# Performance work log

Hardware: AMD Instinct MI355X
Metric: run time of the kernel (lower is better)

Reference implementation:

```python
import jax, jax.numpy as jnp
import numpy as np
import math

H = 1024
N = 64          # d_state; complex modes = N // 2
N2 = N // 2
B = 8
L = 2048
DT_MIN, DT_MAX = 0.001, 0.1


def setup_inputs() -> dict:
    key = jax.random.key(0)
    ks = jax.random.split(key, 8)
    u = jax.random.normal(ks[0], (B, H, L), dtype=jnp.float32)
    # log_dt ~ Uniform[log(dt_min), log(dt_max)]
    log_dt = (jax.random.uniform(ks[1], (H,), dtype=jnp.float32)
              * (math.log(DT_MAX) - math.log(DT_MIN)) + math.log(DT_MIN))
    # random_dplr with scaling='inverse': real part 0.5, imag = (1/pi)*N*(N/(1+2n)-1)
    n = jnp.arange(N2, dtype=jnp.float32)
    w_real = 0.5 * jnp.ones((1, N2), dtype=jnp.float32)
    w_imag = ((1.0 / math.pi) * N * (N / (1.0 + 2.0 * n) - 1.0))[None, :].astype(jnp.float32)
    log_w_real = jnp.log(w_real + 1e-4)  # module stores log(-w.real + 1e-4)
    # C = randn complex (channels=1, H, N2), scaled by normalized B (folded into randn here)
    C_re = jax.random.normal(ks[2], (1, H, N2), dtype=jnp.float32) / math.sqrt(2 * N2)
    C_im = jax.random.normal(ks[3], (1, H, N2), dtype=jnp.float32) / math.sqrt(2 * N2)
    D = jax.random.normal(ks[4], (1, H), dtype=jnp.float32)
    # output_linear: Conv1d(k=1) from channels*H -> H  => weight (H, H)
    W_out = jax.random.normal(ks[5], (H, H), dtype=jnp.float32) / math.sqrt(H)
    b_out = jax.random.normal(ks[6], (H,), dtype=jnp.float32) * 0.01
    return {"u": u, "log_dt": log_dt, "log_w_real": log_w_real, "w_imag": w_imag,
            "C_re": C_re, "C_im": C_im, "D": D, "W_out": W_out, "b_out": b_out}


def reference(u, log_dt, log_w_real, w_imag, C_re, C_im, D, W_out, b_out):
    b, h, l = u.shape
    # --- SSKernelDiag.forward ---
    dt = jnp.exp(log_dt)                                   # (H,)
    w = -jnp.exp(log_w_real) + 1j * w_imag                 # (n_ssm=1, N2)
    w = jnp.broadcast_to(w, (h, w.shape[-1]))              # repeat copies -> (H, N2)
    dtA = w * dt[:, None]                                  # (H, N2) complex
    C = (C_re + 1j * C_im) * (jnp.exp(dtA) - 1.0) / w      # (c, H, N2)
    # Vandermonde: exp(dtA * arange(L)) -> (H, N2, L) complex
    K = jnp.exp(dtA[:, :, None] * jnp.arange(l, dtype=jnp.float32))
    k = 2.0 * jnp.einsum('chn,hnl->chl', C, K).real        # (c, H, L) float
    # --- FFT convolution ---
    k_f = jnp.fft.rfft(k, n=2 * l)                         # (c, H, L+1)
    u_f = jnp.fft.rfft(u, n=2 * l)                         # (B, H, L+1)
    y_f = jnp.einsum('bhl,chl->bchl', u_f, k_f)
    y = jnp.fft.irfft(y_f, n=2 * l)[..., :l]               # (B, c, H, L)
    # skip connection with D
    y = y + jnp.einsum('bhl,ch->bchl', u, D)
    y = y.reshape(b, -1, l)                                # (B, c*H, L)
    y = jax.nn.gelu(y, approximate=False)
    # output 1x1 conv: (B, c*H, L) x (H, c*H) -> (B, H, L)
    y = jnp.einsum('bil,oi->bol', y, W_out) + b_out[None, :, None]
    return y
```

## Files before the change

### kernel.cpp

```cpp
#include <hip/hip_runtime.h>
#include <hip/hip_bf16.h>

#define HH 1024
#define LL 2048
#define BB 8
#define NN2 32
#define CT 128
#define NCH 16

typedef short bf16x8 __attribute__((ext_vector_type(8)));
typedef float f32x4  __attribute__((ext_vector_type(4)));

static __device__ __forceinline__ unsigned short bfbits(float x) {
    __hip_bfloat16 h = __float2bfloat16(x);
    return *(unsigned short*)&h;
}
static __device__ __forceinline__ float f_from_bits(unsigned short b) {
    __hip_bfloat16 h; *(unsigned short*)&h = b; return __bfloat162float(h);
}
static __device__ __forceinline__ float2 cexp_n(float2 dA, float p) {
    float mag = __expf(dA.x * p);
    float rev = dA.y * p * 0.15915494309f;
    rev -= floorf(rev);
    float ang = rev * 6.28318530718f;
    return make_float2(mag * __cosf(ang), mag * __sinf(ang));
}

#define SWZ(off, row) ((off) ^ (((row) & 7) << 4))

__global__ __launch_bounds__(256) void aux_tables(
    const float* __restrict__ log_dt, const float* __restrict__ log_w_real,
    const float* __restrict__ w_imag, const float* __restrict__ C_re,
    const float* __restrict__ C_im,
    __hip_bfloat16* __restrict__ AJ_g, __hip_bfloat16* __restrict__ AP_g,
    float* __restrict__ misc_g)
{
    __shared__ float2 dtA_s[NN2];
    __shared__ float2 Cn_s[NN2];
    const int tid = threadIdx.x;
    const int h = blockIdx.x;

    if (tid < NN2) {
        int n = tid;
        float dt = expf(log_dt[h]);
        float wr = -expf(log_w_real[n]);
        float wi = w_imag[n];
        float dar = wr * dt, dai = wi * dt;
        dtA_s[n] = make_float2(dar, dai);
        float er = expf(dar);
        float sn, cs; sincosf(dai, &sn, &cs);
        float exr = er * cs - 1.0f, exi = er * sn;
        float den = wr * wr + wi * wi;
        float fr = (exr * wr + exi * wi) / den;
        float fi = (exi * wr - exr * wi) / den;
        float cre = C_re[h * NN2 + n], cim = C_im[h * NN2 + n];
        float2 Cv = make_float2(cre * fr - cim * fi, cre * fi + cim * fr);
        Cn_s[n] = Cv;
        misc_g[h * 256 + 128 + 2 * n]     = Cv.x;
        misc_g[h * 256 + 128 + 2 * n + 1] = Cv.y;
        float magA = expf(dar * 128.0f);
        float snA, csA; sincosf(dai * 128.0f, &snA, &csA);
        misc_g[h * 256 + 192 + 2 * n]     = magA * csA;
        misc_g[h * 256 + 192 + 2 * n + 1] = magA * snA;
    }
    __syncthreads();

    char* ajb = (char*)AJ_g + (size_t)h * 16384;
    #pragma unroll
    for (int q = 0; q < 2; ++q) {
        int task = q * 256 + tid;
        int n = task >> 4, j0 = (task & 15) * 8;
        float2 dA = dtA_s[n];
        unsigned rw[4], iw[4];
        #pragma unroll
        for (int i2 = 0; i2 < 4; ++i2) {
            float2 a0 = cexp_n(dA, (float)(127 - j0 - 2 * i2));
            float2 a1 = cexp_n(dA, (float)(127 - j0 - 2 * i2 - 1));
            rw[i2] = (unsigned)bfbits(a0.x) | ((unsigned)bfbits(a1.x) << 16);
            iw[i2] = (unsigned)bfbits(a0.y) | ((unsigned)bfbits(a1.y) << 16);
        }
        int r0 = 2 * n, r1 = 2 * n + 1;
        *(uint4*)(ajb + SWZ(r0 * 256 + j0 * 2, r0)) = make_uint4(rw[0], rw[1], rw[2], rw[3]);
        *(uint4*)(ajb + SWZ(r1 * 256 + j0 * 2, r1)) = make_uint4(iw[0], iw[1], iw[2], iw[3]);
    }

    char* apb = (char*)AP_g + (size_t)h * 16384;
    #pragma unroll
    for (int q = 0; q < 2; ++q) {
        int task = q * 256 + tid;
        int ttr = task >> 2, n0 = (task & 3) * 8;
        unsigned w[8];
        #pragma unroll
        for (int i = 0; i < 8; ++i) {
            float2 a = cexp_n(dtA_s[n0 + i], (float)(ttr + 1));
            w[i] = (unsigned)bfbits(2.0f * a.x) | ((unsigned)bfbits(-2.0f * a.y) << 16);
        }
        *(uint4*)(apb + SWZ(ttr * 128 + n0 * 4, ttr))      = make_uint4(w[0], w[1], w[2], w[3]);
        *(uint4*)(apb + SWZ(ttr * 128 + n0 * 4 + 16, ttr)) = make_uint4(w[4], w[5], w[6], w[7]);
    }

    {
        int t = tid >> 1, nb = (tid & 1) * 16;
        float s = 0.f;
        #pragma unroll
        for (int i = 0; i < 16; ++i) {
            int n = nb + i;
            float2 a = cexp_n(dtA_s[n], (float)t);
            float2 C = Cn_s[n];
            s += C.x * a.x - C.y * a.y;
        }
        s += __shfl_xor(s, 1);
        if ((tid & 1) == 0) misc_g[h * 256 + t] = 2.0f * s;
    }
}

#define S_U    0
#define S_UN   32768
#define S_P    49152
#define S_KT   65536
#define S_TOT  66560

#define KBUILD(hf)                                                       \
    _Pragma("unroll")                                                    \
    for (int q = 0; q < 4; ++q) {                                        \
        int idx = q * 512 + tid;                                         \
        int ttr = idx >> 4, j0 = (idx & 15) * 4;                         \
        int base = ttr - (hf) * 64 - j0;                                 \
        ushort4 o;                                                       \
        o.x = (base     >= 0) ? bfbits(kt[base])     : (unsigned short)0;\
        o.y = (base - 1 >= 0) ? bfbits(kt[base - 1]) : (unsigned short)0;\
        o.z = (base - 2 >= 0) ? bfbits(kt[base - 2]) : (unsigned short)0;\
        o.w = (base - 3 >= 0) ? bfbits(kt[base - 3]) : (unsigned short)0;\
        *(ushort4*)(smem + SWZ(S_UN + ttr * 128 + j0 * 2, ttr)) = o;     \
    }

__global__ __launch_bounds__(512, 4) void ssm_mfma(
    const float* __restrict__ u,
    const __hip_bfloat16* __restrict__ AJ_g,
    const __hip_bfloat16* __restrict__ AP_g,
    const float* __restrict__ misc_g,
    const float* __restrict__ Dp, __hip_bfloat16* __restrict__ g_out)
{
    extern __shared__ char smem[];
    float*  kt   = (float*)(smem + S_KT);
    float2* CnL  = (float2*)(smem + S_KT + 512);
    float2* A128 = (float2*)(smem + S_KT + 768);

    const int tid  = threadIdx.x;
    const int lane = tid & 63;
    const int wave = tid >> 6;
    const int wr4  = wave >> 1;
    const int wc2  = wave & 1;
    const int h    = blockIdx.x;

    {
        const char* ajs = (const char*)AJ_g + (size_t)h * 16384;
        __builtin_amdgcn_global_load_lds(
            (const __attribute__((address_space(1))) void*)(ajs + tid * 16),
            (__attribute__((address_space(3))) void*)(smem + S_UN + wave * 1024), 16, 0, 0);
        __builtin_amdgcn_global_load_lds(
            (const __attribute__((address_space(1))) void*)(ajs + 8192 + tid * 16),
            (__attribute__((address_space(3))) void*)(smem + S_UN + 8192 + wave * 1024), 16, 0, 0);
        if (tid < 64) {
            const char* ms = (const char*)misc_g + (size_t)h * 1024;
            __builtin_amdgcn_global_load_lds(
                (const __attribute__((address_space(1))) void*)(ms + tid * 16),
                (__attribute__((address_space(3))) void*)(smem + S_KT), 16, 0, 0);
        }
    }

    float4 ureg[8];
    #pragma unroll
    for (int q = 0; q < 8; ++q)
        ureg[q] = *(const float4*)(u + ((size_t)(q * HH + h)) * LL + tid * 4);
    #pragma unroll
    for (int q = 0; q < 8; ++q) {
        int row = q * 16 + (tid >> 5);
        int j   = (tid & 31) * 4;
        ushort4 o;
        o.x = bfbits(ureg[q].x); o.y = bfbits(ureg[q].y);
        o.z = bfbits(ureg[q].z); o.w = bfbits(ureg[q].w);
        *(ushort4*)(smem + SWZ(S_U + row * 256 + j * 2, row)) = o;
    }
    asm volatile("s_waitcnt vmcnt(0)" ::: "memory");
    __syncthreads();

    f32x4 accP[2][2] = {};
    #pragma unroll
    for (int ks = 0; ks < 4; ++ks) {
        int kf = ks * 32 + (lane >> 4) * 8;
        bf16x8 a0, a1, b0, b1;
        {
            int r = wr4 * 32 + (lane & 15);
            a0 = *(bf16x8*)(smem + SWZ(S_U + r * 256 + kf * 2, r));
            int r2 = r + 16;
            a1 = *(bf16x8*)(smem + SWZ(S_U + r2 * 256 + kf * 2, r2));
        }
        {
            int r = wc2 * 32 + (lane & 15);
            b0 = *(bf16x8*)(smem + SWZ(S_UN + r * 256 + kf * 2, r));
            int r2 = r + 16;
            b1 = *(bf16x8*)(smem + SWZ(S_UN + r2 * 256 + kf * 2, r2));
        }
        accP[0][0] = __builtin_amdgcn_mfma_f32_16x16x32_bf16(a0, b0, accP[0][0], 0, 0, 0);
        accP[0][1] = __builtin_amdgcn_mfma_f32_16x16x32_bf16(a0, b1, accP[0][1], 0, 0, 0);
        accP[1][0] = __builtin_amdgcn_mfma_f32_16x16x32_bf16(a1, b0, accP[1][0], 0, 0, 0);
        accP[1][1] = __builtin_amdgcn_mfma_f32_16x16x32_bf16(a1, b1, accP[1][1], 0, 0, 0);
    }
    #pragma unroll
    for (int mt = 0; mt < 2; ++mt)
        #pragma unroll
        for (int nt = 0; nt < 2; ++nt)
            #pragma unroll
            for (int r = 0; r < 4; ++r) {
                int row = wr4 * 32 + mt * 16 + (lane >> 4) * 4 + r;
                int col = wc2 * 32 + nt * 16 + (lane & 15);
                *(unsigned short*)(smem + SWZ(S_P + row * 128 + col * 2, row)) =
                    bfbits(accP[mt][nt][r]);
            }
    __syncthreads();

    KBUILD(0)
    if (tid < 256) {
        int b = tid >> 5, n = tid & 31;
        float2 C = CnL[n];
        float2 A = A128[n];
        float sr = 0.f, si = 0.f;
        for (int c = 0; c < NCH; ++c) {
            int row = b * 16 + c;
            int off = SWZ(S_P + row * 128 + n * 4, row);
            unsigned int pv = *(unsigned int*)(smem + off);
            float pr = f_from_bits((unsigned short)(pv & 0xffff));
            float pi = f_from_bits((unsigned short)(pv >> 16));
            float csr = C.x * sr - C.y * si;
            float csi = C.x * si + C.y * sr;
            *(unsigned int*)(smem + off) =
                (unsigned)bfbits(csr) | ((unsigned)bfbits(csi) << 16);
            float nsr = A.x * sr - A.y * si + pr;
            float nsi = A.x * si + A.y * sr + pi;
            sr = nsr; si = nsi;
        }
    }
    __syncthreads();

    f32x4 acc[2][4] = {};
    #pragma unroll
    for (int ks = 0; ks < 2; ++ks) {
        int kf = ks * 32 + (lane >> 4) * 8;
        bf16x8 a0, a1, bv[4];
        {
            int r = wr4 * 32 + (lane & 15);
            a0 = *(bf16x8*)(smem + SWZ(S_U + r * 256 + kf * 2, r));
            int r2 = r + 16;
            a1 = *(bf16x8*)(smem + SWZ(S_U + r2 * 256 + kf * 2, r2));
        }
        #pragma unroll
        for (int nt = 0; nt < 4; ++nt) {
            int ttr = wc2 * 64 + nt * 16 + (lane & 15);
            bv[nt] = *(bf16x8*)(smem + SWZ(S_UN + ttr * 128 + kf * 2, ttr));
        }
        #pragma unroll
        for (int nt = 0; nt < 4; ++nt) {
            acc[0][nt] = __builtin_amdgcn_mfma_f32_16x16x32_bf16(a0, bv[nt], acc[0][nt], 0, 0, 0);
            acc[1][nt] = __builtin_amdgcn_mfma_f32_16x16x32_bf16(a1, bv[nt], acc[1][nt], 0, 0, 0);
        }
    }
    __syncthreads();

    KBUILD(1)
    __syncthreads();
    #pragma unroll
    for (int ks = 0; ks < 2; ++ks) {
        int kf = ks * 32 + (lane >> 4) * 8;
        bf16x8 a0, a1, bv[4];
        {
            int r = wr4 * 32 + (lane & 15);
            a0 = *(bf16x8*)(smem + SWZ(S_U + r * 256 + 128 + kf * 2, r));
            int r2 = r + 16;
            a1 = *(bf16x8*)(smem + SWZ(S_U + r2 * 256 + 128 + kf * 2, r2));
        }
        #pragma unroll
        for (int nt = 0; nt < 4; ++nt) {
            int ttr = wc2 * 64 + nt * 16 + (lane & 15);
            bv[nt] = *(bf16x8*)(smem + SWZ(S_UN + ttr * 128 + kf * 2, ttr));
        }
        #pragma unroll
        for (int nt = 0; nt < 4; ++nt) {
            acc[0][nt] = __builtin_amdgcn_mfma_f32_16x16x32_bf16(a0, bv[nt], acc[0][nt], 0, 0, 0);
            acc[1][nt] = __builtin_amdgcn_mfma_f32_16x16x32_bf16(a1, bv[nt], acc[1][nt], 0, 0, 0);
        }
    }
    __syncthreads();

    {
        const char* aps = (const char*)AP_g + (size_t)h * 16384;
        __builtin_amdgcn_global_load_lds(
            (const __attribute__((address_space(1))) void*)(aps + tid * 16),
            (__attribute__((address_space(3))) void*)(smem + S_UN + wave * 1024), 16, 0, 0);
        __builtin_amdgcn_global_load_lds(
            (const __attribute__((address_space(1))) void*)(aps + 8192 + tid * 16),
            (__attribute__((address_space(3))) void*)(smem + S_UN + 8192 + wave * 1024), 16, 0, 0);
    }
    asm volatile("s_waitcnt vmcnt(0)" ::: "memory");
    __syncthreads();

    #pragma unroll
    for (int ks = 0; ks < 2; ++ks) {
        int kf = ks * 32 + (lane >> 4) * 8;
        bf16x8 a0, a1, bv[4];
        {
            int r = wr4 * 32 + (lane & 15);
            a0 = *(bf16x8*)(smem + SWZ(S_P + r * 128 + kf * 2, r));
            int r2 = r + 16;
            a1 = *(bf16x8*)(smem + SWZ(S_P + r2 * 128 + kf * 2, r2));
        }
        #pragma unroll
        for (int nt = 0; nt < 4; ++nt) {
            int ttr = wc2 * 64 + nt * 16 + (lane & 15);
            bv[nt] = *(bf16x8*)(smem + SWZ(S_UN + ttr * 128 + kf * 2, ttr));
        }
        #pragma unroll
        for (int nt = 0; nt < 4; ++nt) {
            acc[0][nt] = __builtin_amdgcn_mfma_f32_16x16x32_bf16(a0, bv[nt], acc[0][nt], 0, 0, 0);
            acc[1][nt] = __builtin_amdgcn_mfma_f32_16x16x32_bf16(a1, bv[nt], acc[1][nt], 0, 0, 0);
        }
    }

    const float Dv = Dp[h];
    #pragma unroll
    for (int mt = 0; mt < 2; ++mt)
        #pragma unroll
        for (int nt = 0; nt < 4; ++nt)
            #pragma unroll
            for (int r = 0; r < 4; ++r) {
                int row = wr4 * 32 + mt * 16 + (lane >> 4) * 4 + r;
                int ttr = wc2 * 64 + nt * 16 + (lane & 15);
                int off = SWZ(S_U + row * 256 + ttr * 2, row);
                float uv = f_from_bits(*(unsigned short*)(smem + off));
                float y = acc[mt][nt][r] + Dv * uv;
                float z = 0.7978845608f * (y + 0.044715f * y * y * y);
                float e = __expf(2.0f * z);
                float th = 1.0f - 2.0f / (e + 1.0f);
                float gel = 0.5f * y * (1.0f + th);
                *(unsigned short*)(smem + off) = bfbits(gel);
            }
    __syncthreads();
    #pragma unroll
    for (int q = 0; q < 4; ++q) {
        int flat = q * 512 + tid;
        int row = flat >> 4, c16 = flat & 15;
        uint4 v = *(uint4*)(smem + SWZ(S_U + row * 256 + c16 * 16, row));
        int b = row >> 4, c = row & 15;
        *(uint4*)(g_out + ((size_t)(b * HH + h)) * LL + c * CT + c16 * 8) = v;
    }
}

__global__ __launch_bounds__(256) void conv_w(
    const float* __restrict__ W, __hip_bfloat16* __restrict__ Wb)
{
    int i = blockIdx.x * 256 + threadIdx.x;
    float4 v = ((const float4*)W)[i];
    ushort4 o;
    o.x = bfbits(v.x); o.y = bfbits(v.y); o.z = bfbits(v.z); o.w = bfbits(v.w);
    ((ushort4*)Wb)[i] = o;
}

__global__ __launch_bounds__(256) void transpose_g(
    const __hip_bfloat16* __restrict__ g, __hip_bfloat16* __restrict__ gT)
{
    __shared__ __hip_bfloat16 t[64][66];
    const int tid = threadIdx.x;
    const int b  = blockIdx.z;
    const int h0 = blockIdx.x * 64;
    const int l0 = blockIdx.y * 64;

    #pragma unroll
    for (int q = 0; q < 2; ++q) {
        int idx = tid + q * 256;
        int r = idx >> 3, c8 = (idx & 7) * 8;
        uint4 v = *(const uint4*)(g + ((size_t)(b * HH + h0 + r)) * LL + l0 + c8);
        unsigned int* dst = (unsigned int*)&t[r][c8];
        dst[0] = v.x; dst[1] = v.y; dst[2] = v.z; dst[3] = v.w;
    }
    __syncthreads();
    #pragma unroll
    for (int q = 0; q < 2; ++q) {
        int idx = tid + q * 256;
        int r = idx >> 3, c8 = (idx & 7) * 8;
        unsigned short tmp[8];
        #pragma unroll
        for (int j = 0; j < 8; ++j) tmp[j] = *(unsigned short*)&t[c8 + j][r];
        uint4 o;
        o.x = (unsigned)tmp[0] | ((unsigned)tmp[1] << 16);
        o.y = (unsigned)tmp[2] | ((unsigned)tmp[3] << 16);
        o.z = (unsigned)tmp[4] | ((unsigned)tmp[5] << 16);
        o.w = (unsigned)tmp[6] | ((unsigned)tmp[7] << 16);
        *(uint4*)(gT + ((size_t)(b * LL + l0 + r)) * HH + h0 + c8) = o;
    }
}

#define GSLOT 32768
#define STAGE_TILE(kt_, s_)                                                      \
    {                                                                            \
        const int k0_ = (kt_) * 64;                                              \
        _Pragma("unroll")                                                        \
        for (int v_ = 0; v_ < 4; ++v_) {                                         \
            int row_ = v_ * 64 + rsub;                                           \
            const __hip_bfloat16* ga_ = Wb + (size_t)(o0 + row_) * HH + k0_ + csw; \
            const __hip_bfloat16* gb_ = gT + (size_t)(n0 + row_) * HH + k0_ + csw; \
            char* dA_ = smem + (s_) * GSLOT + (v_ * 64 + wave * 8) * 128;        \
            char* dB_ = smem + 2 * GSLOT + (s_) * GSLOT + (v_ * 64 + wave * 8) * 128; \
            __builtin_amdgcn_global_load_lds(                                    \
                (const __attribute__((address_space(1))) void*)ga_,              \
                (__attribute__((address_space(3))) void*)dA_, 16, 0, 0);         \
            __builtin_amdgcn_global_load_lds(                                    \
                (const __attribute__((address_space(1))) void*)gb_,              \
                (__attribute__((address_space(3))) void*)dB_, 16, 0, 0);         \
        }                                                                        \
    }

#define COMPUTE_TILE(s_)                                                         \
    {                                                                            \
        const char* baseA = smem + (s_) * GSLOT;                                 \
        const char* baseB = smem + 2 * GSLOT + (s_) * GSLOT;                     \
        bf16x8 bfr[4][2];                                                        \
        _Pragma("unroll")                                                        \
        for (int nt = 0; nt < 4; ++nt)                                           \
            _Pragma("unroll")                                                    \
            for (int ks = 0; ks < 2; ++ks) {                                     \
                int rb = wn * 64 + nt * 16 + (lane & 15);                        \
                int c  = (ks * 32 + (lane >> 4) * 8) ^ ((rb & 7) << 3);          \
                bfr[nt][ks] = *(const bf16x8*)(baseB + rb * 128 + c * 2);        \
            }                                                                    \
        _Pragma("unroll")                                                        \
        for (int qq = 0; qq < 4; ++qq) {                                         \
            bf16x8 af[2][2];                                                     \
            _Pragma("unroll")                                                    \
            for (int mt = 0; mt < 2; ++mt)                                       \
                _Pragma("unroll")                                                \
                for (int ks = 0; ks < 2; ++ks) {                                 \
                    int ra = wm * 128 + (qq * 2 + mt) * 16 + (lane & 15);        \
                    int c  = (ks * 32 + (lane >> 4) * 8) ^ ((ra & 7) << 3);      \
                    af[mt][ks] = *(const bf16x8*)(baseA + ra * 128 + c * 2);     \
                }                                                                \
            __builtin_amdgcn_s_setprio(1);                                       \
            _Pragma("unroll")                                                    \
            for (int mt = 0; mt < 2; ++mt)                                       \
                _Pragma("unroll")                                                \
                for (int nt = 0; nt < 4; ++nt) {                                 \
                    acc[qq * 2 + mt][nt] = __builtin_amdgcn_mfma_f32_16x16x32_bf16( \
                        af[mt][0], bfr[nt][0], acc[qq * 2 + mt][nt], 0, 0, 0);   \
                    acc[qq * 2 + mt][nt] = __builtin_amdgcn_mfma_f32_16x16x32_bf16( \
                        af[mt][1], bfr[nt][1], acc[qq * 2 + mt][nt], 0, 0, 0);   \
                }                                                                \
            __builtin_amdgcn_s_setprio(0);                                       \
        }                                                                        \
    }

__global__ __launch_bounds__(512, 2) void out_gemm_256(
    const __hip_bfloat16* __restrict__ Wb,
    const __hip_bfloat16* __restrict__ gT,
    const float* __restrict__ bias,
    float* __restrict__ out)
{
    extern __shared__ char smem[];
    const int tid  = threadIdx.x;
    const int lane = tid & 63;
    const int wave = tid >> 6;
    const int wm = wave >> 2;
    const int wn = wave & 3;

    int wg  = blockIdx.x;
    int swz = (wg & 7) * 32 + (wg >> 3);
    const int o0 = (swz & 3) * 256;
    const int n0 = (swz >> 2) * 256;

    const int rsub = tid >> 3;
    const int csw  = ((tid & 7) ^ (rsub & 7)) << 3;

    f32x4 acc[8][4] = {};

    STAGE_TILE(0, 0)
    STAGE_TILE(1, 1)

    for (int t = 0; t < 15; ++t) {
        asm volatile("s_waitcnt vmcnt(8)" ::: "memory");
        __builtin_amdgcn_s_barrier();
        __builtin_amdgcn_sched_barrier(0);
        COMPUTE_TILE(t & 1)
        asm volatile("s_waitcnt lgkmcnt(0)" ::: "memory");
        __builtin_amdgcn_s_barrier();
        __builtin_amdgcn_sched_barrier(0);
        if (t < 14) STAGE_TILE(t + 2, t & 1)
    }
    asm volatile("s_waitcnt vmcnt(0)" ::: "memory");
    __builtin_amdgcn_s_barrier();
    __builtin_amdgcn_sched_barrier(0);
    COMPUTE_TILE(1)

    const int bb = n0 >> 11;
    #pragma unroll
    for (int m = 0; m < 8; ++m) {
        int o = o0 + wm * 128 + m * 16 + (lane >> 4) * 4;
        #pragma unroll
        for (int nt = 0; nt < 4; ++nt) {
            int n = n0 + wn * 64 + nt * 16 + (lane & 15);
            int l = n & 2047;
            #pragma unroll
            for (int r = 0; r < 4; ++r)
                out[((size_t)(bb * HH + o + r)) * LL + l] = acc[m][nt][r] + bias[o + r];
        }
    }
}

extern "C" void kernel_launch(void* const* d_in, const int* in_sizes, int n_in,
                              void* d_out, int out_size, void* d_ws, size_t ws_size,
                              hipStream_t stream) {
    const float* u          = (const float*)d_in[0];
    const float* log_dt     = (const float*)d_in[1];
    const float* log_w_real = (const float*)d_in[2];
    const float* w_imag     = (const float*)d_in[3];
    const float* C_re       = (const float*)d_in[4];
    const float* C_im       = (const float*)d_in[5];
    const float* Dp         = (const float*)d_in[6];
    const float* W          = (const float*)d_in[7];
    const float* bias       = (const float*)d_in[8];
    float* out = (float*)d_out;

    __hip_bfloat16* AJ_g = (__hip_bfloat16*)d_out;
    __hip_bfloat16* AP_g = (__hip_bfloat16*)((char*)d_out + 16777216);
    __hip_bfloat16* g    = (__hip_bfloat16*)((char*)d_out + 33554432);
    __hip_bfloat16* gT     = (__hip_bfloat16*)d_ws;
    __hip_bfloat16* Wb     = (__hip_bfloat16*)((char*)d_ws + 33554432);
    float*          misc_g = (float*)((char*)d_ws + 35651584);

    hipFuncSetAttribute((const void*)ssm_mfma,
                        hipFuncAttributeMaxDynamicSharedMemorySize, S_TOT);
    hipFuncSetAttribute((const void*)out_gemm_256,
                        hipFuncAttributeMaxDynamicSharedMemorySize, 131072);

    conv_w<<<dim3(HH * HH / 1024), 256, 0, stream>>>(W, Wb);
    aux_tables<<<dim3(HH), 256, 0, stream>>>(log_dt, log_w_real, w_imag,
                                             C_re, C_im, AJ_g, AP_g, misc_g);
    ssm_mfma<<<dim3(HH), 512, S_TOT, stream>>>(u, AJ_g, AP_g, misc_g, Dp, g);
    transpose_g<<<dim3(HH / 64, LL / 64, BB), 256, 0, stream>>>(g, gT);
    out_gemm_256<<<dim3(256), 512, 131072, stream>>>(Wb, gT, bias, out);
}
```

Measured before the change: 107.6 us.

## Replace Toeplitz KBUILD with shifted kernel rows, fuse weight conversion, prefetch AP early

Instead of materialising the 128x128 Toeplitz block of the SSM kernel twice (KBUILD for each half), each wave builds one of 8 shifted, reversed copies of the kernel, and the MFMA B operands are read straight from those padded rows. This removes two block-wide syncs and one of the two half passes of the intra-chunk GEMM. The AP_g async global-to-LDS load now starts before the state scan, so it overlaps with that work. The separate fp32-to-bf16 weight conversion kernel is folded into aux_tables, which removes one launch. LDS use grows slightly, and the unswizzled padded-row reads may cause bank conflicts.

```diff
diff --git a/kernel.cpp b/kernel.cpp
--- a/kernel.cpp
+++ b/kernel.cpp
@@ -31,14 +31,21 @@
 __global__ __launch_bounds__(256) void aux_tables(
     const float* __restrict__ log_dt, const float* __restrict__ log_w_real,
     const float* __restrict__ w_imag, const float* __restrict__ C_re,
-    const float* __restrict__ C_im,
+    const float* __restrict__ C_im, const float* __restrict__ W,
     __hip_bfloat16* __restrict__ AJ_g, __hip_bfloat16* __restrict__ AP_g,
-    float* __restrict__ misc_g)
+    float* __restrict__ misc_g, __hip_bfloat16* __restrict__ Wb)
 {
     __shared__ float2 dtA_s[NN2];
     __shared__ float2 Cn_s[NN2];
     const int tid = threadIdx.x;
     const int h = blockIdx.x;
+
+    {
+        float4 v = ((const float4*)(W + (size_t)h * HH))[tid];
+        ushort4 o;
+        o.x = bfbits(v.x); o.y = bfbits(v.y); o.z = bfbits(v.z); o.w = bfbits(v.w);
+        ((ushort4*)(Wb + (size_t)h * HH))[tid] = o;
+    }
 
     if (tid < NN2) {
         int n = tid;
@@ -118,21 +125,8 @@
 #define S_UN   32768
 #define S_P    49152
 #define S_KT   65536
-#define S_TOT  66560
-
-#define KBUILD(hf)                                                       \
-    _Pragma("unroll")                                                    \
-    for (int q = 0; q < 4; ++q) {                                        \
-        int idx = q * 512 + tid;                                         \
-        int ttr = idx >> 4, j0 = (idx & 15) * 4;                         \
-        int base = ttr - (hf) * 64 - j0;                                 \
-        ushort4 o;                                                       \
-        o.x = (base     >= 0) ? bfbits(kt[base])     : (unsigned short)0;\
-        o.y = (base - 1 >= 0) ? bfbits(kt[base - 1]) : (unsigned short)0;\
-        o.z = (base - 2 >= 0) ? bfbits(kt[base - 2]) : (unsigned short)0;\
-        o.w = (base - 3 >= 0) ? bfbits(kt[base - 3]) : (unsigned short)0;\
-        *(ushort4*)(smem + SWZ(S_UN + ttr * 128 + j0 * 2, ttr)) = o;     \
-    }
+#define S_KTP  66560
+#define S_TOT  70784
 
 __global__ __launch_bounds__(512, 4) void ssm_mfma(
     const float* __restrict__ u,
@@ -185,6 +179,21 @@
     asm volatile("s_waitcnt vmcnt(0)" ::: "memory");
     __syncthreads();
 
+    {
+        int s = wave;
+        int i0 = lane * 4;
+        ushort4 o;
+        #pragma unroll
+        for (int k = 0; k < 4; ++k) {
+            int src = 127 - s - (i0 + k);
+            ((unsigned short*)&o)[k] = (src >= 0) ? bfbits(kt[src]) : (unsigned short)0;
+        }
+        *(ushort4*)(smem + S_KTP + s * 528 + i0 * 2) = o;
+        if (lane < 2) {
+            *(ushort4*)(smem + S_KTP + s * 528 + 512 + lane * 8) = make_ushort4(0, 0, 0, 0);
+        }
+    }
+
     f32x4 accP[2][2] = {};
     #pragma unroll
     for (int ks = 0; ks < 4; ++ks) {
@@ -220,7 +229,16 @@
             }
     __syncthreads();
 
-    KBUILD(0)
+    {
+        const char* aps = (const char*)AP_g + (size_t)h * 16384;
+        __builtin_amdgcn_global_load_lds(
+            (const __attribute__((address_space(1))) void*)(aps + tid * 16),
+            (__attribute__((address_space(3))) void*)(smem + S_UN + wave * 1024), 16, 0, 0);
+        __builtin_amdgcn_global_load_lds(
+            (const __attribute__((address_space(1))) void*)(aps + 8192 + tid * 16),
+            (__attribute__((address_space(3))) void*)(smem + S_UN + 8192 + wave * 1024), 16, 0, 0);
+    }
+
     if (tid < 256) {
         int b = tid >> 5, n = tid & 31;
         float2 C = CnL[n];
@@ -241,11 +259,10 @@
             sr = nsr; si = nsi;
         }
     }
-    __syncthreads();
 
     f32x4 acc[2][4] = {};
     #pragma unroll
-    for (int ks = 0; ks < 2; ++ks) {
+    for (int ks = 0; ks < 4; ++ks) {
         int kf = ks * 32 + (lane >> 4) * 8;
         bf16x8 a0, a1, bv[4];
         {
@@ -257,49 +274,15 @@
         #pragma unroll
         for (int nt = 0; nt < 4; ++nt) {
             int ttr = wc2 * 64 + nt * 16 + (lane & 15);
-            bv[nt] = *(bf16x8*)(smem + SWZ(S_UN + ttr * 128 + kf * 2, ttr));
+            int s   = (127 - ttr) & 7;
+            int gq  = (127 - ttr + kf) >> 3;
+            bv[nt] = *(bf16x8*)(smem + S_KTP + s * 528 + gq * 16);
         }
         #pragma unroll
         for (int nt = 0; nt < 4; ++nt) {
             acc[0][nt] = __builtin_amdgcn_mfma_f32_16x16x32_bf16(a0, bv[nt], acc[0][nt], 0, 0, 0);
             acc[1][nt] = __builtin_amdgcn_mfma_f32_16x16x32_bf16(a1, bv[nt], acc[1][nt], 0, 0, 0);
         }
-    }
-    __syncthreads();
-
-    KBUILD(1)
-    __syncthreads();
-    #pragma unroll
-    for (int ks = 0; ks < 2; ++ks) {
-        int kf = ks * 32 + (lane >> 4) * 8;
-        bf16x8 a0, a1, bv[4];
-        {
-            int r = wr4 * 32 + (lane & 15);
-            a0 = *(bf16x8*)(smem + SWZ(S_U + r * 256 + 128 + kf * 2, r));
-            int r2 = r + 16;
-            a1 = *(bf16x8*)(smem + SWZ(S_U + r2 * 256 + 128 + kf * 2, r2));
-        }
-        #pragma unroll
-        for (int nt = 0; nt < 4; ++nt) {
-            int ttr = wc2 * 64 + nt * 16 + (lane & 15);
-            bv[nt] = *(bf16x8*)(smem + SWZ(S_UN + ttr * 128 + kf * 2, ttr));
-        }
-        #pragma unroll
-        for (int nt = 0; nt < 4; ++nt) {
-            acc[0][nt] = __builtin_amdgcn_mfma_f32_16x16x32_bf16(a0, bv[nt], acc[0][nt], 0, 0, 0);
-            acc[1][nt] = __builtin_amdgcn_mfma_f32_16x16x32_bf16(a1, bv[nt], acc[1][nt], 0, 0, 0);
-        }
-    }
-    __syncthreads();
-
-    {
-        const char* aps = (const char*)AP_g + (size_t)h * 16384;
-        __builtin_amdgcn_global_load_lds(
-            (const __attribute__((address_space(1))) void*)(aps + tid * 16),
-            (__attribute__((address_space(3))) void*)(smem + S_UN + wave * 1024), 16, 0, 0);
-        __builtin_amdgcn_global_load_lds(
-            (const __attribute__((address_space(1))) void*)(aps + 8192 + tid * 16),
-            (__attribute__((address_space(3))) void*)(smem + S_UN + 8192 + wave * 1024), 16, 0, 0);
     }
     asm volatile("s_waitcnt vmcnt(0)" ::: "memory");
     __syncthreads();
@@ -353,16 +336,6 @@
         int b = row >> 4, c = row & 15;
         *(uint4*)(g_out + ((size_t)(b * HH + h)) * LL + c * CT + c16 * 8) = v;
     }
-}
-
-__global__ __launch_bounds__(256) void conv_w(
-    const float* __restrict__ W, __hip_bfloat16* __restrict__ Wb)
-{
-    int i = blockIdx.x * 256 + threadIdx.x;
-    float4 v = ((const float4*)W)[i];
-    ushort4 o;
-    o.x = bfbits(v.x); o.y = bfbits(v.y); o.z = bfbits(v.z); o.w = bfbits(v.w);
-    ((ushort4*)Wb)[i] = o;
 }
 
 __global__ __launch_bounds__(256) void transpose_g(
@@ -539,9 +512,8 @@
     hipFuncSetAttribute((const void*)out_gemm_256,
                         hipFuncAttributeMaxDynamicSharedMemorySize, 131072);
 
-    conv_w<<<dim3(HH * HH / 1024), 256, 0, stream>>>(W, Wb);
     aux_tables<<<dim3(HH), 256, 0, stream>>>(log_dt, log_w_real, w_imag,
-                                             C_re, C_im, AJ_g, AP_g, misc_g);
+                                             C_re, C_im, W, AJ_g, AP_g, misc_g, Wb);
     ssm_mfma<<<dim3(HH), 512, S_TOT, stream>>>(u, AJ_g, AP_g, misc_g, Dp, g);
     transpose_g<<<dim3(HH / 64, LL / 64, BB), 256, 0, stream>>>(g, gT);
     out_gemm_256<<<dim3(256), 512, 131072, stream>>>(Wb, gT, bias, out);
```

New measurement: 104.6 us. 2.8% less time.
